# Kernel optimization log

Measured on AMD Instinct MI355X. Metric: run time of the kernel, lower is better.

Reference implementation:

```python
import jax, jax.numpy as jnp
import numpy as np

N, D = 256, 512
DIST_W, ANGLE_W = 1.0, 2.0
EPS_PD = 1e-6    # F.pairwise_distance eps (added to the difference)
EPS_COS = 1e-8   # F.cosine_similarity eps (denominator floor)
CLAMP = 1e-7     # acos clamp margin


def _smooth_l1(x):
    # F.smooth_l1_loss with beta=1.0, elementwise (reduction handled by caller)
    ax = jnp.abs(x)
    return jnp.where(ax < 1.0, 0.5 * ax * ax, ax - 0.5)


def _pairwise_dist(E):
    # Faithful to the looped version: dist[i,j] = ||e_i - e_j + eps|| for i<j,
    # mirrored to the lower triangle, zero diagonal.
    diff = E[:, None, :] - E[None, :, :] + EPS_PD          # [n, n, d]
    d = jnp.sqrt(jnp.sum(diff * diff, axis=-1))            # [n, n]
    upper = jnp.triu(d, k=1)
    return upper + upper.T


def _angles(E):
    # ang[j, i, k] = angle at vertex j between (e_i - e_j) and (e_k - e_j)
    Dv = E[None, :, :] - E[:, None, :]                     # Dv[j, a] = e_a - e_j
    norms = jnp.sqrt(jnp.sum(Dv * Dv, axis=-1))            # [n, n]
    dots = jnp.einsum('jad,jbd->jab', Dv, Dv)              # [n, n, n]
    denom = jnp.maximum(norms[:, :, None] * norms[:, None, :], EPS_COS)
    cos = jnp.clip(dots / denom, -1.0 + CLAMP, 1.0 - CLAMP)
    return jnp.arccos(cos)


def setup_inputs() -> dict:
    key = jax.random.key(0)
    k1, k2 = jax.random.split(key)
    return {
        'student_embeddings': jax.random.normal(k1, (N, D), dtype=jnp.float32),
        'teacher_embeddings': jax.random.normal(k2, (N, D), dtype=jnp.float32),
    }


def reference(student_embeddings, teacher_embeddings):
    # distance-wise loss: smooth_l1 mean over the full n x n matrix
    ds = _pairwise_dist(student_embeddings)
    dt = _pairwise_dist(teacher_embeddings)
    distance_loss = jnp.mean(_smooth_l1(ds - dt))

    # angle-wise loss: mean over triplets i<j<k (vertex at j)
    n = student_embeddings.shape[0]
    ang_s = _angles(student_embeddings)
    ang_t = _angles(teacher_embeddings)
    idx = jnp.arange(n)
    # mask[j, i, k] = (i < j) & (j < k)
    mask = (idx[None, :, None] < idx[:, None, None]) & (idx[:, None, None] < idx[None, None, :])
    count = n * (n - 1) * (n - 2) // 6
    angle_loss = jnp.sum(_smooth_l1(ang_s - ang_t) * mask) / count

    total_loss = DIST_W * distance_loss + ANGLE_W * angle_loss
    return (total_loss, distance_loss, angle_loss)
```

## Files before the change

kernel.cpp:

```cpp
#include <hip/hip_runtime.h>
#include <math.h>

#define N 256
#define D 512
#define SPLIT 4

using f32x4  = __attribute__((ext_vector_type(4))) float;
using bf16x8 = __attribute__((ext_vector_type(8))) short;

__device__ __forceinline__ short f2bf(float f) {
    unsigned u = __float_as_uint(f);
    u += 0x7fffu + ((u >> 16) & 1u);
    return (short)(u >> 16);
}

__device__ __forceinline__ float smooth_l1(float x) {
    float ax = fabsf(x);
    return ax < 1.f ? 0.5f * ax * ax : ax - 0.5f;
}

__device__ __forceinline__ float acos_fast(float x) {
    float ax = fabsf(x);
    float p = -0.0187293f;
    p = p * ax + 0.0742610f;
    p = p * ax - 0.2121144f;
    p = p * ax + 1.5707288f;
    float v = sqrtf(1.f - ax) * p;
    return x < 0.f ? 3.14159265358979f - v : v;
}

__global__ __launch_bounds__(64) void gram_kernel(const float* __restrict__ Es,
                                                  const float* __restrict__ Et,
                                                  float2* __restrict__ G2,
                                                  float* __restrict__ acc) {
    const int lane = threadIdx.x;
    if (blockIdx.x == 0 && blockIdx.y == 0 && blockIdx.z == 0 && lane == 0) {
        acc[0] = 0.f;
        acc[1] = 0.f;
    }
    const float* E = blockIdx.z ? Et : Es;
    const int m = lane & 15, quad = lane >> 4;
    const int baseA = (blockIdx.y * 16 + m) * D + quad * 8;
    const int baseB = (blockIdx.x * 16 + m) * D + quad * 8;

    f32x4 c = {0.f, 0.f, 0.f, 0.f};
#pragma unroll
    for (int k0 = 0; k0 < D; k0 += 32) {
        float4 alo = *(const float4*)&E[baseA + k0];
        float4 ahi = *(const float4*)&E[baseA + k0 + 4];
        float4 blo = *(const float4*)&E[baseB + k0];
        float4 bhi = *(const float4*)&E[baseB + k0 + 4];
        bf16x8 a, b;
        a[0] = f2bf(alo.x); a[1] = f2bf(alo.y); a[2] = f2bf(alo.z); a[3] = f2bf(alo.w);
        a[4] = f2bf(ahi.x); a[5] = f2bf(ahi.y); a[6] = f2bf(ahi.z); a[7] = f2bf(ahi.w);
        b[0] = f2bf(blo.x); b[1] = f2bf(blo.y); b[2] = f2bf(blo.z); b[3] = f2bf(blo.w);
        b[4] = f2bf(bhi.x); b[5] = f2bf(bhi.y); b[6] = f2bf(bhi.z); b[7] = f2bf(bhi.w);
        c = __builtin_amdgcn_mfma_f32_16x16x32_bf16(a, b, c, 0, 0, 0);
    }

    const int col = blockIdx.x * 16 + m;
#pragma unroll
    for (int r = 0; r < 4; ++r) {
        const int row = blockIdx.y * 16 + quad * 4 + r;
        float* slot = (float*)&G2[row * N + col];
        slot[blockIdx.z] = c[r];
    }
}

__global__ __launch_bounds__(256) void angle_dist_kernel(const float2* __restrict__ G2,
                                                         float* __restrict__ acc) {
    const int j = blockIdx.x + 1;
    const int tid = threadIdx.x;
    __shared__ float2 sv[N], tv[N];
    __shared__ float2 red[256];
    const float2 gjj = G2[j * N + j];
    const float Gsjj = gjj.x, Gtjj = gjj.y;

    float distp = 0.f;
    {
        const int a = tid;
        float2 gaj = G2[a * N + j];
        float2 gaa = G2[a * N + a];
        float n2s = gaa.x - 2.f * gaj.x + Gsjj;
        float n2t = gaa.y - 2.f * gaj.y + Gtjj;
        float rs = (a == j) ? 0.f : rsqrtf(n2s);
        float rt = (a == j) ? 0.f : rsqrtf(n2t);
        sv[a] = make_float2(gaj.x, rs);
        tv[a] = make_float2(gaj.y, rt);
        if (blockIdx.y == 0 && a < j)
            distp = smooth_l1(n2s * rs - n2t * rt);
    }
    __syncthreads();

    const int nk = 255 - j;
    const int npairs = j * nk;
    const float inv_nk = 1.0f / (float)nk;
    const float lo = -0.99999994f;
    const float hi = 0.99999994f;

    float anglep = 0.f;
    for (int p = blockIdx.y * 256 + tid; p < npairs; p += 256 * SPLIT) {
        int i = (int)((float)p * inv_nk);
        int rem = p - i * nk;
        if (rem < 0) { --i; rem += nk; }
        else if (rem >= nk) { ++i; rem -= nk; }
        const int k = j + 1 + rem;
        float2 si = sv[i], sk = sv[k];
        float2 ti = tv[i], tk = tv[k];
        float2 gik = G2[i * N + k];
        float dots = gik.x - si.x - sk.x + Gsjj;
        float dott = gik.y - ti.x - tk.x + Gtjj;
        float coss = fminf(fmaxf(dots * (si.y * sk.y), lo), hi);
        float cost = fminf(fmaxf(dott * (ti.y * tk.y), lo), hi);
        anglep += smooth_l1(acos_fast(coss) - acos_fast(cost));
    }

    red[tid] = make_float2(distp, anglep);
    __syncthreads();
    for (int s = 128; s > 0; s >>= 1) {
        if (tid < s) {
            red[tid].x += red[tid + s].x;
            red[tid].y += red[tid + s].y;
        }
        __syncthreads();
    }
    if (tid == 0) {
        atomicAdd(&acc[1], red[0].y);
        if (blockIdx.y == 0) atomicAdd(&acc[0], red[0].x);
    }
}

__global__ void finalize_kernel(const float* __restrict__ acc,
                                float* __restrict__ out) {
    float dl = 2.f * acc[0] / (float)(N * N);
    float al = acc[1] / (float)(N * (N - 1) * (N - 2) / 6);
    out[0] = 1.0f * dl + 2.0f * al;
    out[1] = dl;
    out[2] = al;
}

extern "C" void kernel_launch(void* const* d_in, const int* in_sizes, int n_in,
                              void* d_out, int out_size, void* d_ws, size_t ws_size,
                              hipStream_t stream) {
    const float* Es = (const float*)d_in[0];
    const float* Et = (const float*)d_in[1];
    float* out = (float*)d_out;
    float* ws = (float*)d_ws;

    float* acc = ws;
    float2* G2 = (float2*)(ws + 64);

    gram_kernel<<<dim3(16, 16, 2), 64, 0, stream>>>(Es, Et, G2, acc);
    angle_dist_kernel<<<dim3(N - 1, SPLIT), 256, 0, stream>>>(G2, acc);
    finalize_kernel<<<1, 1, 0, stream>>>(acc, out);
}
```

Measured before the change: 86.22 us.

## Fuse gram, angle and finalize kernels into one cooperative kernel with grid syncs

```diff
diff --git a/kernel.cpp b/kernel.cpp
--- a/kernel.cpp
+++ b/kernel.cpp
@@ -1,9 +1,13 @@
 #include <hip/hip_runtime.h>
+#include <hip/hip_cooperative_groups.h>
 #include <math.h>
+
+namespace cg = cooperative_groups;
 
 #define N 256
 #define D 512
 #define SPLIT 4
+#define NBLK ((N - 1) * SPLIT)
 
 using f32x4  = __attribute__((ext_vector_type(4))) float;
 using bf16x8 = __attribute__((ext_vector_type(8))) short;
@@ -29,114 +33,129 @@
     return x < 0.f ? 3.14159265358979f - v : v;
 }
 
-__global__ __launch_bounds__(64) void gram_kernel(const float* __restrict__ Es,
-                                                  const float* __restrict__ Et,
-                                                  float2* __restrict__ G2,
-                                                  float* __restrict__ acc) {
-    const int lane = threadIdx.x;
-    if (blockIdx.x == 0 && blockIdx.y == 0 && blockIdx.z == 0 && lane == 0) {
+__global__ __launch_bounds__(256, 4) void rkd_fused_kernel(const float* __restrict__ Es,
+                                                           const float* __restrict__ Et,
+                                                           float2* __restrict__ G2,
+                                                           float* __restrict__ acc,
+                                                           float* __restrict__ out) {
+    cg::grid_group grid = cg::this_grid();
+    const int tid = threadIdx.x;
+    const int bid = blockIdx.x;
+
+    __shared__ float2 sv[N], tv[N];
+    __shared__ float2 red[256];
+
+    if (bid == 0 && tid == 0) {
         acc[0] = 0.f;
         acc[1] = 0.f;
     }
-    const float* E = blockIdx.z ? Et : Es;
-    const int m = lane & 15, quad = lane >> 4;
-    const int baseA = (blockIdx.y * 16 + m) * D + quad * 8;
-    const int baseB = (blockIdx.x * 16 + m) * D + quad * 8;
 
-    f32x4 c = {0.f, 0.f, 0.f, 0.f};
+    {
+        const int gw = bid * 4 + (tid >> 6);
+        if (gw < 512) {
+            const int z = gw >> 8;
+            const int tile = gw & 255;
+            const int by = tile >> 4, bx = tile & 15;
+            const float* E = z ? Et : Es;
+            const int lane = tid & 63;
+            const int m = lane & 15, quad = lane >> 4;
+            const int baseA = (by * 16 + m) * D + quad * 8;
+            const int baseB = (bx * 16 + m) * D + quad * 8;
+
+            f32x4 c = {0.f, 0.f, 0.f, 0.f};
 #pragma unroll
-    for (int k0 = 0; k0 < D; k0 += 32) {
-        float4 alo = *(const float4*)&E[baseA + k0];
-        float4 ahi = *(const float4*)&E[baseA + k0 + 4];
-        float4 blo = *(const float4*)&E[baseB + k0];
-        float4 bhi = *(const float4*)&E[baseB + k0 + 4];
-        bf16x8 a, b;
-        a[0] = f2bf(alo.x); a[1] = f2bf(alo.y); a[2] = f2bf(alo.z); a[3] = f2bf(alo.w);
-        a[4] = f2bf(ahi.x); a[5] = f2bf(ahi.y); a[6] = f2bf(ahi.z); a[7] = f2bf(ahi.w);
-        b[0] = f2bf(blo.x); b[1] = f2bf(blo.y); b[2] = f2bf(blo.z); b[3] = f2bf(blo.w);
-        b[4] = f2bf(bhi.x); b[5] = f2bf(bhi.y); b[6] = f2bf(bhi.z); b[7] = f2bf(bhi.w);
-        c = __builtin_amdgcn_mfma_f32_16x16x32_bf16(a, b, c, 0, 0, 0);
+            for (int k0 = 0; k0 < D; k0 += 32) {
+                float4 alo = *(const float4*)&E[baseA + k0];
+                float4 ahi = *(const float4*)&E[baseA + k0 + 4];
+                float4 blo = *(const float4*)&E[baseB + k0];
+                float4 bhi = *(const float4*)&E[baseB + k0 + 4];
+                bf16x8 a, b;
+                a[0] = f2bf(alo.x); a[1] = f2bf(alo.y); a[2] = f2bf(alo.z); a[3] = f2bf(alo.w);
+                a[4] = f2bf(ahi.x); a[5] = f2bf(ahi.y); a[6] = f2bf(ahi.z); a[7] = f2bf(ahi.w);
+                b[0] = f2bf(blo.x); b[1] = f2bf(blo.y); b[2] = f2bf(blo.z); b[3] = f2bf(blo.w);
+                b[4] = f2bf(bhi.x); b[5] = f2bf(bhi.y); b[6] = f2bf(bhi.z); b[7] = f2bf(bhi.w);
+                c = __builtin_amdgcn_mfma_f32_16x16x32_bf16(a, b, c, 0, 0, 0);
+            }
+            const int col = bx * 16 + m;
+#pragma unroll
+            for (int r = 0; r < 4; ++r) {
+                const int row = by * 16 + quad * 4 + r;
+                ((float*)&G2[row * N + col])[z] = c[r];
+            }
+        }
     }
 
-    const int col = blockIdx.x * 16 + m;
-#pragma unroll
-    for (int r = 0; r < 4; ++r) {
-        const int row = blockIdx.y * 16 + quad * 4 + r;
-        float* slot = (float*)&G2[row * N + col];
-        slot[blockIdx.z] = c[r];
-    }
-}
+    grid.sync();
 
-__global__ __launch_bounds__(256) void angle_dist_kernel(const float2* __restrict__ G2,
-                                                         float* __restrict__ acc) {
-    const int j = blockIdx.x + 1;
-    const int tid = threadIdx.x;
-    __shared__ float2 sv[N], tv[N];
-    __shared__ float2 red[256];
-    const float2 gjj = G2[j * N + j];
-    const float Gsjj = gjj.x, Gtjj = gjj.y;
+    {
+        const int j = (bid % (N - 1)) + 1;
+        const int sp = bid / (N - 1);
+        const float2 gjj = G2[j * N + j];
+        const float Gsjj = gjj.x, Gtjj = gjj.y;
 
-    float distp = 0.f;
-    {
-        const int a = tid;
-        float2 gaj = G2[a * N + j];
-        float2 gaa = G2[a * N + a];
-        float n2s = gaa.x - 2.f * gaj.x + Gsjj;
-        float n2t = gaa.y - 2.f * gaj.y + Gtjj;
-        float rs = (a == j) ? 0.f : rsqrtf(n2s);
-        float rt = (a == j) ? 0.f : rsqrtf(n2t);
-        sv[a] = make_float2(gaj.x, rs);
-        tv[a] = make_float2(gaj.y, rt);
-        if (blockIdx.y == 0 && a < j)
-            distp = smooth_l1(n2s * rs - n2t * rt);
-    }
-    __syncthreads();
+        float distp = 0.f;
+        {
+            const int a = tid;
+            float2 gaj = G2[a * N + j];
+            float2 gaa = G2[a * N + a];
+            float n2s = gaa.x - 2.f * gaj.x + Gsjj;
+            float n2t = gaa.y - 2.f * gaj.y + Gtjj;
+            float rs = (a == j) ? 0.f : rsqrtf(n2s);
+            float rt = (a == j) ? 0.f : rsqrtf(n2t);
+            sv[a] = make_float2(gaj.x, rs);
+            tv[a] = make_float2(gaj.y, rt);
+            if (sp == 0 && a < j)
+                distp = smooth_l1(n2s * rs - n2t * rt);
+        }
+        __syncthreads();
 
-    const int nk = 255 - j;
-    const int npairs = j * nk;
-    const float inv_nk = 1.0f / (float)nk;
-    const float lo = -0.99999994f;
-    const float hi = 0.99999994f;
+        const int nk = 255 - j;
+        const int npairs = j * nk;
+        const float inv_nk = 1.0f / (float)nk;
+        const float lo = -0.99999994f;
+        const float hi = 0.99999994f;
 
-    float anglep = 0.f;
-    for (int p = blockIdx.y * 256 + tid; p < npairs; p += 256 * SPLIT) {
-        int i = (int)((float)p * inv_nk);
-        int rem = p - i * nk;
-        if (rem < 0) { --i; rem += nk; }
-        else if (rem >= nk) { ++i; rem -= nk; }
-        const int k = j + 1 + rem;
-        float2 si = sv[i], sk = sv[k];
-        float2 ti = tv[i], tk = tv[k];
-        float2 gik = G2[i * N + k];
-        float dots = gik.x - si.x - sk.x + Gsjj;
-        float dott = gik.y - ti.x - tk.x + Gtjj;
-        float coss = fminf(fmaxf(dots * (si.y * sk.y), lo), hi);
-        float cost = fminf(fmaxf(dott * (ti.y * tk.y), lo), hi);
-        anglep += smooth_l1(acos_fast(coss) - acos_fast(cost));
+        float anglep = 0.f;
+        for (int p = sp * 256 + tid; p < npairs; p += 256 * SPLIT) {
+            int i = (int)((float)p * inv_nk);
+            int rem = p - i * nk;
+            if (rem < 0) { --i; rem += nk; }
+            else if (rem >= nk) { ++i; rem -= nk; }
+            const int k = j + 1 + rem;
+            float2 si = sv[i], sk = sv[k];
+            float2 ti = tv[i], tk = tv[k];
+            float2 gik = G2[i * N + k];
+            float dots = gik.x - si.x - sk.x + Gsjj;
+            float dott = gik.y - ti.x - tk.x + Gtjj;
+            float coss = fminf(fmaxf(dots * (si.y * sk.y), lo), hi);
+            float cost = fminf(fmaxf(dott * (ti.y * tk.y), lo), hi);
+            anglep += smooth_l1(acos_fast(coss) - acos_fast(cost));
+        }
+
+        red[tid] = make_float2(distp, anglep);
+        __syncthreads();
+        for (int s = 128; s > 0; s >>= 1) {
+            if (tid < s) {
+                red[tid].x += red[tid + s].x;
+                red[tid].y += red[tid + s].y;
+            }
+            __syncthreads();
+        }
+        if (tid == 0) {
+            atomicAdd(&acc[1], red[0].y);
+            if (sp == 0) atomicAdd(&acc[0], red[0].x);
+        }
     }
 
-    red[tid] = make_float2(distp, anglep);
-    __syncthreads();
-    for (int s = 128; s > 0; s >>= 1) {
-        if (tid < s) {
-            red[tid].x += red[tid + s].x;
-            red[tid].y += red[tid + s].y;
-        }
-        __syncthreads();
+    grid.sync();
+
+    if (bid == 0 && tid == 0) {
+        float dl = 2.f * acc[0] / (float)(N * N);
+        float al = acc[1] / (float)(N * (N - 1) * (N - 2) / 6);
+        out[0] = 1.0f * dl + 2.0f * al;
+        out[1] = dl;
+        out[2] = al;
     }
-    if (tid == 0) {
-        atomicAdd(&acc[1], red[0].y);
-        if (blockIdx.y == 0) atomicAdd(&acc[0], red[0].x);
-    }
-}
-
-__global__ void finalize_kernel(const float* __restrict__ acc,
-                                float* __restrict__ out) {
-    float dl = 2.f * acc[0] / (float)(N * N);
-    float al = acc[1] / (float)(N * (N - 1) * (N - 2) / 6);
-    out[0] = 1.0f * dl + 2.0f * al;
-    out[1] = dl;
-    out[2] = al;
 }
 
 extern "C" void kernel_launch(void* const* d_in, const int* in_sizes, int n_in,
@@ -150,7 +169,7 @@
     float* acc = ws;
     float2* G2 = (float2*)(ws + 64);
 
-    gram_kernel<<<dim3(16, 16, 2), 64, 0, stream>>>(Es, Et, G2, acc);
-    angle_dist_kernel<<<dim3(N - 1, SPLIT), 256, 0, stream>>>(G2, acc);
-    finalize_kernel<<<1, 1, 0, stream>>>(acc, out);
+    void* args[] = {(void*)&Es, (void*)&Et, (void*)&G2, (void*)&acc, (void*)&out};
+    hipLaunchCooperativeKernel((void*)rkd_fused_kernel, dim3(NBLK), dim3(256),
+                               args, 0, stream);
 }
```

Measured after the change: 260.5 us. +202.2%, slower.
